# Performance work log

Hardware: AMD Instinct MI355X
Metric: run time of the kernel (lower is better)

Reference implementation:

```python
import jax, jax.numpy as jnp
import numpy as np

B, D, E, N = 2048, 4096, 512, 8192
BN_EPS = 1e-5
COS_EPS = 1e-8


def setup_inputs() -> dict:
    key = jax.random.key(0)
    k1, k2, k3, k4, k5 = jax.random.split(key, 5)
    vf = jax.random.normal(k1, (B, D), dtype=jnp.float32)
    p_wfs = jax.random.normal(k2, (B, D), dtype=jnp.float32)
    n_wfs = jax.random.normal(k3, (N, E), dtype=jnp.float32)
    # BatchNorm1d(4096) affine params (default init gamma=1, beta=0; use random-ish gamma for generality)
    gamma = jnp.ones((D,), dtype=jnp.float32)
    beta = jnp.zeros((D,), dtype=jnp.float32)
    # Linear(D -> E)
    lim = 1.0 / np.sqrt(D)
    W = jax.random.uniform(k4, (E, D), dtype=jnp.float32, minval=-lim, maxval=lim)
    b = jax.random.uniform(k5, (E,), dtype=jnp.float32, minval=-lim, maxval=lim)
    return {"vf": vf, "p_wfs": p_wfs, "n_wfs": n_wfs, "gamma": gamma, "beta": beta, "W": W, "b": b}


def _row_normalize(x, eps=COS_EPS):
    nrm = jnp.sqrt(jnp.sum(x * x, axis=-1, keepdims=True))
    return x / jnp.maximum(nrm, eps)


def reference(vf, p_wfs, n_wfs, gamma, beta, W, b):
    # BatchNorm1d in training mode: batch mean / biased variance over the batch dim
    mean = jnp.mean(vf, axis=0)
    var = jnp.mean((vf - mean) ** 2, axis=0)
    vfn = (vf - mean) * (gamma / jnp.sqrt(var + BN_EPS)) + beta  # [B, D]

    # Linear + ReLU embedding
    emb = jax.nn.relu(vfn @ W.T + b)  # [B, E]

    # p_e: row-wise cosine(normed vf, p_wfs) -> [B]
    p_e = jnp.sum(_row_normalize(vfn) * _row_normalize(p_wfs), axis=-1)

    # n_e: cosine(emb[v], n_wfs[n]) for all v,n -> one normalized GEMM [B, N]
    n_e = _row_normalize(emb) @ _row_normalize(n_wfs).T

    n_neg = n_wfs.shape[0]
    n_e_stack = n_e.reshape(-1, 1)                      # [B*N, 1]
    p_e_stack = jnp.repeat(p_e, n_neg).reshape(-1, 1)   # [B*N, 1], p_e[v] repeated N times
    return (n_e_stack, p_e_stack)
```

## Files before the change

### kernel.cpp

```cpp
#include <hip/hip_runtime.h>
#include <stdint.h>
#include <stddef.h>

#define B_ 2048
#define D_ 4096
#define E_ 512
#define N_ 8192
#define SPLITK 4

typedef unsigned short ushort_t;
typedef __attribute__((ext_vector_type(8))) short short8;
typedef __attribute__((ext_vector_type(4))) float floatx4;
typedef __attribute__((ext_vector_type(4))) unsigned short ushort4_t;

__device__ __forceinline__ void async_load16(const void* g, void* l) {
  __builtin_amdgcn_global_load_lds((__attribute__((address_space(1))) void*)(g),
                                   (__attribute__((address_space(3))) void*)(l), 16, 0, 0);
}

__device__ __forceinline__ ushort_t f2bf(float f) {
  unsigned int u = __float_as_uint(f);
  unsigned int r = (u + 0x7fffu + ((u >> 16) & 1u)) >> 16;
  return (ushort_t)r;
}
__device__ __forceinline__ float bf2f(ushort_t h) {
  return __uint_as_float(((unsigned int)h) << 16);
}

__global__ __launch_bounds__(256) void bn_partial(const float* __restrict__ vf,
                                                  float* __restrict__ psum,
                                                  float* __restrict__ psq) {
  int d4 = blockIdx.x * 256 + threadIdx.x;
  int chunk = blockIdx.y;
  floatx4 s = {0.f, 0.f, 0.f, 0.f}, q = {0.f, 0.f, 0.f, 0.f};
  int r0 = chunk * 32;
  for (int r = r0; r < r0 + 32; ++r) {
    floatx4 v = ((const floatx4*)(vf + (size_t)r * D_))[d4];
    s += v; q += v * v;
  }
  ((floatx4*)(psum + (size_t)chunk * D_))[d4] = s;
  ((floatx4*)(psq  + (size_t)chunk * D_))[d4] = q;
}

__global__ __launch_bounds__(256) void prep_all(const float* __restrict__ psum,
                                                const float* __restrict__ psq,
                                                const float* __restrict__ gamma,
                                                const float* __restrict__ beta,
                                                const float* __restrict__ W,
                                                const float* __restrict__ nw,
                                                float* __restrict__ scale,
                                                float* __restrict__ shift,
                                                ushort_t* __restrict__ wb,
                                                ushort_t* __restrict__ nwb,
                                                float* __restrict__ inv_nw) {
  int bid = blockIdx.x;
  if (bid < 4) {
    int d4 = bid * 256 + threadIdx.x;
    floatx4 s = {0.f, 0.f, 0.f, 0.f}, q = {0.f, 0.f, 0.f, 0.f};
    for (int c = 0; c < 64; ++c) {
      s += ((const floatx4*)(psum + (size_t)c * D_))[d4];
      q += ((const floatx4*)(psq  + (size_t)c * D_))[d4];
    }
    floatx4 g = ((const floatx4*)gamma)[d4];
    floatx4 bt = ((const floatx4*)beta)[d4];
    floatx4 sc, sh;
#pragma unroll
    for (int j = 0; j < 4; ++j) {
      float mean = s[j] * (1.0f / B_);
      float var  = q[j] * (1.0f / B_) - mean * mean;
      float scj  = g[j] * rsqrtf(var + 1e-5f);
      sc[j] = scj;
      sh[j] = bt[j] - mean * scj;
    }
    ((floatx4*)scale)[d4] = sc;
    ((floatx4*)shift)[d4] = sh;
  } else if (bid < 2052) {
    size_t i = ((size_t)(bid - 4) * 256 + threadIdx.x) * 4;
    floatx4 x = *(const floatx4*)(W + i);
    ushort4_t o;
#pragma unroll
    for (int j = 0; j < 4; ++j) o[j] = f2bf(x[j]);
    *(ushort4_t*)(wb + i) = o;
  } else {
    int wv = threadIdx.x >> 6, l = threadIdx.x & 63;
    int n = (bid - 2052) * 4 + wv;
    const floatx4* src = (const floatx4*)(nw + (size_t)n * E_);
    ushort4_t* dst = (ushort4_t*)(nwb + (size_t)n * E_);
    float s = 0.f;
#pragma unroll
    for (int k = 0; k < 2; ++k) {
      floatx4 x = src[l + 64 * k];
      ushort4_t o;
#pragma unroll
      for (int j = 0; j < 4; ++j) { o[j] = f2bf(x[j]); s += x[j] * x[j]; }
      dst[l + 64 * k] = o;
    }
    for (int off = 32; off; off >>= 1) s += __shfl_down(s, off);
    if (l == 0) inv_nw[n] = 1.f / fmaxf(sqrtf(s), 1e-8f);
  }
}

__global__ __launch_bounds__(256) void pe_cast(const float* __restrict__ vf,
                                               const float* __restrict__ p,
                                               const float* __restrict__ scale,
                                               const float* __restrict__ shift,
                                               ushort_t* __restrict__ vfn,
                                               float* __restrict__ pe) {
  int wv = threadIdx.x >> 6, l = threadIdx.x & 63;
  int v = blockIdx.x * 4 + wv;
  const floatx4* vf4 = (const floatx4*)(vf + (size_t)v * D_);
  const floatx4* p4  = (const floatx4*)(p  + (size_t)v * D_);
  const floatx4* sc4 = (const floatx4*)scale;
  const floatx4* sh4 = (const floatx4*)shift;
  ushort_t* vrow = vfn + (size_t)v * D_;
  float sd = 0.f, sa = 0.f, sb = 0.f;
#pragma unroll 4
  for (int k = 0; k < 16; ++k) {
    int i = l + 64 * k;
    floatx4 x = vf4[i], y = p4[i], s = sc4[i], t = sh4[i];
    ushort4_t o;
#pragma unroll
    for (int j = 0; j < 4; ++j) {
      float xn = x[j] * s[j] + t[j];
      o[j] = f2bf(xn);
      sd += xn * y[j]; sa += xn * xn; sb += y[j] * y[j];
    }
    *(ushort4_t*)(vrow + i * 4) = o;
  }
  for (int off = 32; off; off >>= 1) {
    sd += __shfl_down(sd, off); sa += __shfl_down(sa, off); sb += __shfl_down(sb, off);
  }
  if (l == 0) {
    float na = fmaxf(sqrtf(sa), 1e-8f), nb = fmaxf(sqrtf(sb), 1e-8f);
    pe[v] = sd / (na * nb);
  }
}

template <int BM, int BN, int BK, int WCOLS, int MT, int NT>
__device__ __forceinline__ void gemm_core(const ushort_t* __restrict__ A,
                                          const ushort_t* __restrict__ Bt, int K,
                                          int kb, int ke, int bm0, int bn0,
                                          ushort_t* As, ushort_t* Bs,
                                          floatx4 (&acc)[MT][NT]) {
  const int tid = threadIdx.x, w = tid >> 6, l = tid & 63;
  constexpr int ISS_A = BM * BK / 2048;
  constexpr int ISS_B = BN * BK / 2048;
  const int wr = w / WCOLS, wc = w % WCOLS;
  const int m16 = l & 15, q = l >> 4;

  for (int k0 = kb; k0 < ke; k0 += BK) {
#pragma unroll
    for (int i = 0; i < ISS_A; ++i) {
      int e = i * 2048 + tid * 8;
      int row = e / BK, col = e % BK;
      async_load16(A + (size_t)(bm0 + row) * K + (k0 + col), &As[i * 2048 + w * 512]);
    }
#pragma unroll
    for (int i = 0; i < ISS_B; ++i) {
      int e = i * 2048 + tid * 8;
      int row = e / BK, col = e % BK;
      async_load16(Bt + (size_t)(bn0 + row) * K + (k0 + col), &Bs[i * 2048 + w * 512]);
    }
    __syncthreads();
#pragma unroll
    for (int kc = 0; kc < BK / 32; ++kc) {
      short8 af[MT], bf[NT];
#pragma unroll
      for (int i = 0; i < MT; ++i)
        af[i] = *(const short8*)&As[(wr * (MT * 16) + i * 16 + m16) * BK + kc * 32 + q * 8];
#pragma unroll
      for (int j = 0; j < NT; ++j)
        bf[j] = *(const short8*)&Bs[(wc * (NT * 16) + j * 16 + m16) * BK + kc * 32 + q * 8];
#pragma unroll
      for (int i = 0; i < MT; ++i)
#pragma unroll
        for (int j = 0; j < NT; ++j)
          acc[i][j] = __builtin_amdgcn_mfma_f32_16x16x32_bf16(af[i], bf[j], acc[i][j], 0, 0, 0);
    }
    __syncthreads();
  }
}

__global__ __launch_bounds__(256, 2) void gemm1_splitk(const ushort_t* __restrict__ A,
                                                       const ushort_t* __restrict__ Bt,
                                                       float* __restrict__ partial) {
  __shared__ __align__(16) ushort_t As[128 * 64];
  __shared__ __align__(16) ushort_t Bs[64 * 64];
  floatx4 acc[4][2] = {};
  int bm0 = blockIdx.y * 128, bn0 = blockIdx.x * 64, s = blockIdx.z;
  int kb = s * (D_ / SPLITK);
  gemm_core<128, 64, 64, 2, 4, 2>(A, Bt, D_, kb, kb + D_ / SPLITK, bm0, bn0, As, Bs, acc);
  int tid = threadIdx.x, w = tid >> 6, l = tid & 63, m16 = l & 15, q = l >> 4;
  int wr = w >> 1, wc = w & 1;
  float* out = partial + (size_t)s * B_ * E_;
#pragma unroll
  for (int i = 0; i < 4; ++i)
#pragma unroll
    for (int j = 0; j < 2; ++j) {
      int col = bn0 + wc * 32 + j * 16 + m16;
#pragma unroll
      for (int r = 0; r < 4; ++r) {
        int row = bm0 + wr * 64 + i * 16 + q * 4 + r;
        out[(size_t)row * E_ + col] = acc[i][j][r];
      }
    }
}

__global__ __launch_bounds__(256) void gemm1_reduce(const float* __restrict__ partial,
                                                    const float* __restrict__ bias,
                                                    ushort_t* __restrict__ emb,
                                                    float* __restrict__ inv_emb) {
  int wv = threadIdx.x >> 6, l = threadIdx.x & 63;
  int row = blockIdx.x * 4 + wv;
  float sumsq = 0.f;
#pragma unroll
  for (int k = 0; k < 2; ++k) {
    int i = l + 64 * k;
    floatx4 v = {0.f, 0.f, 0.f, 0.f};
#pragma unroll
    for (int s = 0; s < SPLITK; ++s)
      v += ((const floatx4*)(partial + (size_t)s * B_ * E_ + (size_t)row * E_))[i];
    floatx4 bb = ((const floatx4*)bias)[i];
    ushort4_t o;
#pragma unroll
    for (int j = 0; j < 4; ++j) {
      float f = fmaxf(v[j] + bb[j], 0.f);
      o[j] = f2bf(f);
      float fb = bf2f(o[j]);
      sumsq += fb * fb;
    }
    ((ushort4_t*)(emb + (size_t)row * E_))[i] = o;
  }
  for (int off = 32; off; off >>= 1) sumsq += __shfl_down(sumsq, off);
  if (l == 0) inv_emb[row] = 1.f / fmaxf(sqrtf(sumsq), 1e-8f);
}

__global__ __launch_bounds__(256, 2) void gemm2_kernel(const ushort_t* __restrict__ A,
                                                       const ushort_t* __restrict__ Bt,
                                                       const float* __restrict__ inv_a,
                                                       const float* __restrict__ inv_b,
                                                       const float* __restrict__ pe,
                                                       float* __restrict__ out) {
  __shared__ __align__(16) ushort_t As[128 * 64];
  __shared__ __align__(16) ushort_t Bs[128 * 64];
  floatx4 acc[4][4] = {};
  const int tid = threadIdx.x, w = tid >> 6, l = tid & 63;
  const int m16 = l & 15, q = l >> 4;
  const int wr = w >> 1, wc = w & 1;
  const int bm0 = blockIdx.y * 128, bn0 = blockIdx.x * 128;

  float pv[4][4];
#pragma unroll
  for (int i = 0; i < 4; ++i)
#pragma unroll
    for (int r = 0; r < 4; ++r)
      pv[i][r] = pe[bm0 + wr * 64 + i * 16 + q * 4 + r];
  float* out2lane = out + (size_t)B_ * N_ + bn0 + wc * 64 + m16;

#pragma unroll
  for (int it = 0; it < E_ / 64; ++it) {
    int k0 = it * 64;
#pragma unroll
    for (int i = 0; i < 4; ++i) {
      int e = i * 2048 + tid * 8;
      async_load16(A + (size_t)(bm0 + e / 64) * E_ + (k0 + e % 64), &As[i * 2048 + w * 512]);
    }
#pragma unroll
    for (int i = 0; i < 4; ++i) {
      int e = i * 2048 + tid * 8;
      async_load16(Bt + (size_t)(bn0 + e / 64) * E_ + (k0 + e % 64), &Bs[i * 2048 + w * 512]);
    }
    __syncthreads();
#pragma unroll
    for (int t = 0; t < 8; ++t) {
      int idx = it * 8 + t;
      int i = idx >> 4, r = (idx >> 2) & 3, j = idx & 3;
      int row = bm0 + wr * 64 + i * 16 + q * 4 + r;
      out2lane[(size_t)row * N_ + j * 16] = pv[i][r];
    }
#pragma unroll
    for (int kc = 0; kc < 2; ++kc) {
      short8 af[4], bf[4];
#pragma unroll
      for (int i = 0; i < 4; ++i)
        af[i] = *(const short8*)&As[(wr * 64 + i * 16 + m16) * 64 + kc * 32 + q * 8];
#pragma unroll
      for (int j = 0; j < 4; ++j)
        bf[j] = *(const short8*)&Bs[(wc * 64 + j * 16 + m16) * 64 + kc * 32 + q * 8];
#pragma unroll
      for (int i = 0; i < 4; ++i)
#pragma unroll
        for (int j = 0; j < 4; ++j)
          acc[i][j] = __builtin_amdgcn_mfma_f32_16x16x32_bf16(af[i], bf[j], acc[i][j], 0, 0, 0);
    }
    __syncthreads();
  }

  float ibv[4];
#pragma unroll
  for (int j = 0; j < 4; ++j) ibv[j] = inv_b[bn0 + wc * 64 + j * 16 + m16];
#pragma unroll
  for (int i = 0; i < 4; ++i)
#pragma unroll
    for (int r = 0; r < 4; ++r) {
      int row = bm0 + wr * 64 + i * 16 + q * 4 + r;
      float ia = inv_a[row];
      size_t base = (size_t)row * N_ + bn0 + wc * 64 + m16;
#pragma unroll
      for (int j = 0; j < 4; ++j)
        out[base + j * 16] = acc[i][j][r] * ia * ibv[j];
    }
}

extern "C" void kernel_launch(void* const* d_in, const int* in_sizes, int n_in,
                              void* d_out, int out_size, void* d_ws, size_t ws_size,
                              hipStream_t stream) {
  (void)in_sizes; (void)n_in; (void)out_size; (void)ws_size;
  const float* vf    = (const float*)d_in[0];
  const float* p_wfs = (const float*)d_in[1];
  const float* n_wfs = (const float*)d_in[2];
  const float* gamma = (const float*)d_in[3];
  const float* beta  = (const float*)d_in[4];
  const float* W     = (const float*)d_in[5];
  const float* bias  = (const float*)d_in[6];
  float* out = (float*)d_out;

  char* ws = (char*)d_ws;
  float* psum    = (float*)ws;  ws += (size_t)64 * D_ * 4;
  float* psq     = (float*)ws;  ws += (size_t)64 * D_ * 4;
  float* scale   = (float*)ws;  ws += (size_t)D_ * 4;
  float* shift   = (float*)ws;  ws += (size_t)D_ * 4;
  float* pe      = (float*)ws;  ws += (size_t)B_ * 4;
  float* inv_nw  = (float*)ws;  ws += (size_t)N_ * 4;
  float* inv_emb = (float*)ws;  ws += (size_t)B_ * 4;
  float* partial = (float*)ws;  ws += (size_t)SPLITK * B_ * E_ * 4;
  ushort_t* vfn  = (ushort_t*)ws;  ws += (size_t)B_ * D_ * 2;
  ushort_t* wb   = (ushort_t*)ws;  ws += (size_t)E_ * D_ * 2;
  ushort_t* nwb  = (ushort_t*)ws;  ws += (size_t)N_ * E_ * 2;
  ushort_t* emb  = (ushort_t*)ws;  ws += (size_t)B_ * E_ * 2;

  bn_partial<<<dim3(D_ / 1024, 64), 256, 0, stream>>>(vf, psum, psq);
  prep_all<<<4 + 2048 + N_ / 4, 256, 0, stream>>>(psum, psq, gamma, beta, W, n_wfs,
                                                  scale, shift, wb, nwb, inv_nw);
  pe_cast<<<B_ / 4, 256, 0, stream>>>(vf, p_wfs, scale, shift, vfn, pe);
  gemm1_splitk<<<dim3(E_ / 64, B_ / 128, SPLITK), 256, 0, stream>>>(vfn, wb, partial);
  gemm1_reduce<<<B_ / 4, 256, 0, stream>>>(partial, bias, emb, inv_emb);
  gemm2_kernel<<<dim3(N_ / 128, B_ / 128), 256, 0, stream>>>(emb, nwb, inv_emb, inv_nw, pe, out);
}
```

Baseline: 271.9 us.

## Rewrite second GEMM as 256x256 tile, 8-wave, double-buffered phased pipeline

Replaces the 128x128 single-buffered GEMM2 kernel with a 256x256 tile kernel using 8 waves. It double-buffers LDS, uses XOR-swizzled layouts to avoid bank conflicts, and splits each K-step into four sub-phases that interleave async global-to-LDS staging with MFMA work. The broadcast p_e writes become vectorized float4 stores sourced via readlane. The aim is to hide load latency and raise data reuse in the output-write-heavy GEMM, at the cost of 128KB of LDS per block and higher register pressure, which may limit occupancy.

```diff
diff --git a/kernel.cpp b/kernel.cpp
--- a/kernel.cpp
+++ b/kernel.cpp
@@ -235,81 +235,161 @@
   if (l == 0) inv_emb[row] = 1.f / fmaxf(sqrtf(sumsq), 1e-8f);
 }
 
-__global__ __launch_bounds__(256, 2) void gemm2_kernel(const ushort_t* __restrict__ A,
-                                                       const ushort_t* __restrict__ Bt,
-                                                       const float* __restrict__ inv_a,
-                                                       const float* __restrict__ inv_b,
-                                                       const float* __restrict__ pe,
-                                                       float* __restrict__ out) {
-  __shared__ __align__(16) ushort_t As[128 * 64];
-  __shared__ __align__(16) ushort_t Bs[128 * 64];
-  floatx4 acc[4][4] = {};
+#define BAR() asm volatile("s_barrier" ::: "memory")
+#define VMW(n) asm volatile("s_waitcnt vmcnt(" #n ")" ::: "memory")
+
+__device__ __forceinline__ void stage_A2(const ushort_t* __restrict__ A, ushort_t* Abuf,
+                                         int bm0, int tk, int h, int tid) {
+#pragma unroll
+  for (int j = 0; j < 2; ++j) {
+    int off = j * 8192 + tid * 16;
+    int sl = off >> 7;
+    int cb = off & 127;
+    int r  = ((sl >> 6) & 1) * 128 + h * 64 + (sl & 63);
+    int cg = cb ^ ((sl & 7) << 4);
+    async_load16(A + (size_t)(bm0 + r) * E_ + tk * 64 + (cg >> 1),
+                 Abuf + h * 8192 + j * 4096 + (tid >> 6) * 512);
+  }
+}
+
+__device__ __forceinline__ void stage_B2(const ushort_t* __restrict__ Bt, ushort_t* Bbuf,
+                                         int bn0, int tk, int h, int tid) {
+#pragma unroll
+  for (int j = 0; j < 2; ++j) {
+    int off = j * 8192 + tid * 16;
+    int sl = off >> 7;
+    int cb = off & 127;
+    int r  = ((sl >> 5) & 3) * 64 + h * 32 + (sl & 31);
+    int cg = cb ^ ((sl & 7) << 4);
+    async_load16(Bt + (size_t)(bn0 + r) * E_ + tk * 64 + (cg >> 1),
+                 Bbuf + h * 8192 + j * 4096 + (tid >> 6) * 512);
+  }
+}
+
+template <int MH, int NH>
+__device__ __forceinline__ void ph_loads(const ushort_t* Ab, const ushort_t* Bb,
+                                         int wr, int wc, int m16, int co0, int co1,
+                                         short8 (&af)[4][2], short8 (&bfr)[2][2]) {
+#pragma unroll
+  for (int f = 0; f < 4; ++f) {
+    const ushort_t* p = Ab + (MH * 128 + wr * 64 + f * 16 + m16) * 64;
+    af[f][0] = *(const short8*)(p + co0);
+    af[f][1] = *(const short8*)(p + co1);
+  }
+#pragma unroll
+  for (int g = 0; g < 2; ++g) {
+    const ushort_t* p = Bb + (NH * 128 + wc * 32 + g * 16 + m16) * 64;
+    bfr[g][0] = *(const short8*)(p + co0);
+    bfr[g][1] = *(const short8*)(p + co1);
+  }
+}
+
+template <int MH, int NH>
+__device__ __forceinline__ void ph_mma(const short8 (&af)[4][2], const short8 (&bfr)[2][2],
+                                       floatx4 (&acc)[2][2][4][2]) {
+  __builtin_amdgcn_s_setprio(1);
+#pragma unroll
+  for (int kc = 0; kc < 2; ++kc)
+#pragma unroll
+    for (int f = 0; f < 4; ++f)
+#pragma unroll
+      for (int g = 0; g < 2; ++g)
+        acc[MH][NH][f][g] =
+            __builtin_amdgcn_mfma_f32_16x16x32_bf16(af[f][kc], bfr[g][kc], acc[MH][NH][f][g], 0, 0, 0);
+  __builtin_amdgcn_s_setprio(0);
+}
+
+__device__ __forceinline__ void out2_batch(float* __restrict__ out2, float pew,
+                                           int bm0, int bn0, int b, int w, int l) {
+#pragma unroll
+  for (int rr = 0; rr < 4; ++rr) {
+    float v = __uint_as_float(__builtin_amdgcn_readlane(__float_as_uint(pew), b * 4 + rr));
+    int row = bm0 + w * 32 + b * 4 + rr;
+    floatx4 vv = {v, v, v, v};
+    *(floatx4*)(out2 + (size_t)row * N_ + bn0 + (l << 2)) = vv;
+  }
+}
+
+#define PH(MH, NH, AB, BB, STAGE, WAIT) \
+  { short8 af[4][2]; short8 bfr[2][2];                                  \
+    ph_loads<MH, NH>(AB, BB, wr, wc, m16, co0, co1, af, bfr);           \
+    STAGE; WAIT;                                                        \
+    BAR();                                                              \
+    ph_mma<MH, NH>(af, bfr, acc);                                       \
+    BAR(); }
+
+__global__ __launch_bounds__(512, 2) void gemm2_8ph(const ushort_t* __restrict__ A,
+                                                    const ushort_t* __restrict__ Bt,
+                                                    const float* __restrict__ inv_a,
+                                                    const float* __restrict__ inv_b,
+                                                    const float* __restrict__ pe,
+                                                    float* __restrict__ out) {
+  __shared__ __align__(16) ushort_t As_[2][16384];
+  __shared__ __align__(16) ushort_t Bs_[2][16384];
   const int tid = threadIdx.x, w = tid >> 6, l = tid & 63;
   const int m16 = l & 15, q = l >> 4;
-  const int wr = w >> 1, wc = w & 1;
-  const int bm0 = blockIdx.y * 128, bn0 = blockIdx.x * 128;
-
-  float pv[4][4];
-#pragma unroll
-  for (int i = 0; i < 4; ++i)
-#pragma unroll
-    for (int r = 0; r < 4; ++r)
-      pv[i][r] = pe[bm0 + wr * 64 + i * 16 + q * 4 + r];
-  float* out2lane = out + (size_t)B_ * N_ + bn0 + wc * 64 + m16;
-
-#pragma unroll
-  for (int it = 0; it < E_ / 64; ++it) {
-    int k0 = it * 64;
-#pragma unroll
-    for (int i = 0; i < 4; ++i) {
-      int e = i * 2048 + tid * 8;
-      async_load16(A + (size_t)(bm0 + e / 64) * E_ + (k0 + e % 64), &As[i * 2048 + w * 512]);
-    }
-#pragma unroll
-    for (int i = 0; i < 4; ++i) {
-      int e = i * 2048 + tid * 8;
-      async_load16(Bt + (size_t)(bn0 + e / 64) * E_ + (k0 + e % 64), &Bs[i * 2048 + w * 512]);
-    }
-    __syncthreads();
-#pragma unroll
-    for (int t = 0; t < 8; ++t) {
-      int idx = it * 8 + t;
-      int i = idx >> 4, r = (idx >> 2) & 3, j = idx & 3;
-      int row = bm0 + wr * 64 + i * 16 + q * 4 + r;
-      out2lane[(size_t)row * N_ + j * 16] = pv[i][r];
-    }
-#pragma unroll
-    for (int kc = 0; kc < 2; ++kc) {
-      short8 af[4], bf[4];
-#pragma unroll
-      for (int i = 0; i < 4; ++i)
-        af[i] = *(const short8*)&As[(wr * 64 + i * 16 + m16) * 64 + kc * 32 + q * 8];
-#pragma unroll
-      for (int j = 0; j < 4; ++j)
-        bf[j] = *(const short8*)&Bs[(wc * 64 + j * 16 + m16) * 64 + kc * 32 + q * 8];
-#pragma unroll
-      for (int i = 0; i < 4; ++i)
-#pragma unroll
-        for (int j = 0; j < 4; ++j)
-          acc[i][j] = __builtin_amdgcn_mfma_f32_16x16x32_bf16(af[i], bf[j], acc[i][j], 0, 0, 0);
-    }
-    __syncthreads();
-  }
-
-  float ibv[4];
-#pragma unroll
-  for (int j = 0; j < 4; ++j) ibv[j] = inv_b[bn0 + wc * 64 + j * 16 + m16];
-#pragma unroll
-  for (int i = 0; i < 4; ++i)
-#pragma unroll
-    for (int r = 0; r < 4; ++r) {
-      int row = bm0 + wr * 64 + i * 16 + q * 4 + r;
-      float ia = inv_a[row];
-      size_t base = (size_t)row * N_ + bn0 + wc * 64 + m16;
-#pragma unroll
-      for (int j = 0; j < 4; ++j)
-        out[base + j * 16] = acc[i][j][r] * ia * ibv[j];
-    }
+  const int wr = w >> 2, wc = w & 3;
+  const int bm0 = blockIdx.y * 256, bn0 = blockIdx.x * 256;
+  const int swz = (m16 & 7) << 4;
+  const int co0 = ((q * 16) ^ swz) >> 1;
+  const int co1 = ((64 + q * 16) ^ swz) >> 1;
+  float* out2 = out + (size_t)B_ * N_;
+
+  floatx4 acc[2][2][4][2] = {};
+
+  float pew = pe[bm0 + w * 32 + (l & 31)];
+  VMW(0);
+
+  stage_A2(A, As_[0], bm0, 0, 0, tid);
+  stage_A2(A, As_[0], bm0, 0, 1, tid);
+  stage_B2(Bt, Bs_[0], bn0, 0, 0, tid);
+  stage_B2(Bt, Bs_[0], bn0, 0, 1, tid);
+  stage_A2(A, As_[1], bm0, 1, 0, tid);
+  stage_B2(Bt, Bs_[1], bn0, 1, 0, tid);
+  VMW(4);
+  BAR();
+
+#pragma unroll
+  for (int i = 0; i < 4; ++i) {
+    const int t1 = 2 * i + 1, t2 = 2 * i + 2, t3 = 2 * i + 3;
+    const bool pre = (i < 3);
+    out2_batch(out2, pew, bm0, bn0, 2 * i, w, l);
+    PH(0, 0, As_[0], Bs_[0], stage_A2(A, As_[1], bm0, t1, 1, tid), ;)
+    PH(0, 1, As_[0], Bs_[0], stage_B2(Bt, Bs_[1], bn0, t1, 1, tid), ;)
+    PH(1, 0, As_[0], Bs_[0], if (pre) stage_A2(A, As_[0], bm0, t2, 0, tid), ;)
+    PH(1, 1, As_[0], Bs_[0],
+       if (pre) stage_B2(Bt, Bs_[0], bn0, t2, 0, tid),
+       if (pre) { VMW(4); } else { VMW(0); })
+    out2_batch(out2, pew, bm0, bn0, 2 * i + 1, w, l);
+    PH(0, 0, As_[1], Bs_[1], if (pre) stage_A2(A, As_[0], bm0, t2, 1, tid), ;)
+    PH(0, 1, As_[1], Bs_[1], if (pre) stage_B2(Bt, Bs_[0], bn0, t2, 1, tid), ;)
+    PH(1, 0, As_[1], Bs_[1], if (pre) stage_A2(A, As_[1], bm0, t3, 0, tid), ;)
+    PH(1, 1, As_[1], Bs_[1],
+       if (pre) stage_B2(Bt, Bs_[1], bn0, t3, 0, tid),
+       if (pre) { VMW(4); })
+  }
+
+  float ibv[2][2];
+#pragma unroll
+  for (int nh = 0; nh < 2; ++nh)
+#pragma unroll
+    for (int g = 0; g < 2; ++g)
+      ibv[nh][g] = inv_b[bn0 + wc * 64 + nh * 32 + g * 16 + m16];
+#pragma unroll
+  for (int mh = 0; mh < 2; ++mh)
+#pragma unroll
+    for (int f = 0; f < 4; ++f)
+#pragma unroll
+      for (int rr = 0; rr < 4; ++rr) {
+        int row = bm0 + wr * 128 + mh * 64 + f * 16 + q * 4 + rr;
+        float ia = inv_a[row];
+        size_t base = (size_t)row * N_ + bn0 + wc * 64;
+#pragma unroll
+        for (int nh = 0; nh < 2; ++nh)
+#pragma unroll
+          for (int g = 0; g < 2; ++g)
+            out[base + nh * 32 + g * 16 + m16] = acc[mh][nh][f][g][rr] * ia * ibv[nh][g];
+      }
 }
 
 extern "C" void kernel_launch(void* const* d_in, const int* in_sizes, int n_in,
@@ -345,5 +425,5 @@
   pe_cast<<<B_ / 4, 256, 0, stream>>>(vf, p_wfs, scale, shift, vfn, pe);
   gemm1_splitk<<<dim3(E_ / 64, B_ / 128, SPLITK), 256, 0, stream>>>(vfn, wb, partial);
   gemm1_reduce<<<B_ / 4, 256, 0, stream>>>(partial, bias, emb, inv_emb);
-  gemm2_kernel<<<dim3(N_ / 128, B_ / 128), 256, 0, stream>>>(emb, nwb, inv_emb, inv_nw, pe, out);
-}
+  gemm2_8ph<<<dim3(N_ / 256, B_ / 256), 512, 0, stream>>>(emb, nwb, inv_emb, inv_nw, pe, out);
+}
```

After: 271.7 us. No clear change (-0.1%).
